# Kernel tuning notes

Measured on AMD Instinct MI355X. Metric: run time of the kernel, lower is better.

Reference implementation:

```python
import jax, jax.numpy as jnp
import numpy as np
from jax import lax

EPS = 1e-5

def _layernorm(x, g, b):
    m = x.mean(-1, keepdims=True)
    v = ((x - m) ** 2).mean(-1, keepdims=True)
    return (x - m) * lax.rsqrt(v + EPS) * g + b

def _batchnorm(x, g, b):
    # x: [N, C, L]; training-mode batch statistics (torch BatchNorm1d default)
    m = x.mean((0, 2), keepdims=True)
    v = ((x - m) ** 2).mean((0, 2), keepdims=True)
    return (x - m) * lax.rsqrt(v + EPS) * g[None, :, None] + b[None, :, None]

def _conv1d(x, w, bias, stride):
    y = lax.conv_general_dilated(x, w, window_strides=(stride,), padding='VALID',
                                 dimension_numbers=('NCH', 'OIH', 'NCH'))
    return y + bias[None, :, None]

def setup_inputs() -> dict:
    key = jax.random.key(0)
    ks = jax.random.split(key, 22)
    B, C, L = 512, 12, 5000
    NF, HID, LAT = 32, 64, 32
    def w(k, shape, fan_in):
        return jax.random.normal(k, shape, jnp.float32) * (1.0 / np.sqrt(fan_in))
    return {
        'x': jax.random.normal(ks[0], (B, C, L), jnp.float32),
        'c1w': w(ks[1], (32, C, 50), C * 50), 'c1b': jnp.zeros((32,), jnp.float32),
        'bn1g': jnp.ones((32,), jnp.float32), 'bn1b': jnp.zeros((32,), jnp.float32),
        'c2w': w(ks[2], (NF, 32, 25), 32 * 25), 'c2b': jnp.zeros((NF,), jnp.float32),
        'bn2g': jnp.ones((NF,), jnp.float32), 'bn2b': jnp.zeros((NF,), jnp.float32),
        'Wi': w(ks[3], (LAT, NF), NF) * 0.5, 'bi': jnp.zeros((LAT,), jnp.float32),
        'ln1g': jnp.ones((LAT,), jnp.float32), 'ln1b': jnp.zeros((LAT,), jnp.float32),
        'Wh': w(ks[4], (HID, LAT), LAT) * 0.5, 'bh': jnp.zeros((HID,), jnp.float32),
        'ln2g': jnp.ones((HID,), jnp.float32), 'ln2b': jnp.zeros((HID,), jnp.float32),
        'Wr': w(ks[5], (LAT, HID), HID) * 0.5, 'br': jnp.zeros((LAT,), jnp.float32),
        'Wo': w(ks[6], (LAT, LAT), LAT), 'bo': jnp.zeros((LAT,), jnp.float32),
    }

def reference(x, c1w, c1b, bn1g, bn1b, c2w, c2b, bn2g, bn2b,
              Wi, bi, ln1g, ln1b, Wh, bh, ln2g, ln2b, Wr, br, Wo, bo):
    # CNN front-end: [B,12,5000] -> [B,32,496] -> [B,32,95]
    h = jax.nn.relu(_batchnorm(_conv1d(x, c1w, c1b, 10), bn1g, bn1b))
    h = jax.nn.relu(_batchnorm(_conv1d(h, c2w, c2b, 5), bn2g, bn2b))
    feats = h.transpose(2, 0, 1)  # [T, B, NF]
    # input_proj + ln1 have no dependence on the recurrent state -> hoist out of loop
    xt_all = _layernorm(jnp.einsum('tbf,lf->tbl', feats, Wi) + bi, ln1g, ln1b)  # [T,B,LAT]

    def step(hstate, xt):
        combined = xt + hstate
        hp = jax.nn.relu(combined @ Wh.T + bh)      # [B, HID]
        hp = _layernorm(hp, ln2g, ln2b)
        hnew = jnp.tanh(hp @ Wr.T + br)             # [B, LAT]
        return hnew, hnew

    h0 = jnp.zeros((x.shape[0], Wr.shape[0]), x.dtype)
    _, outs = lax.scan(step, h0, xt_all)            # outs: [T, B, LAT]
    pooled = outs.mean(0)                           # mean over time
    return pooled @ Wo.T + bo                       # [B, LAT]
```

## Files before the change

### kernel.cpp

```cpp
#include <hip/hip_runtime.h>

#define EPS 1e-5f

#define B    512
#define C_IN 12
#define L_IN 5000
#define C1   32
#define L1   496
#define NF   32
#define L2   95
#define LAT  32
#define HID  64
#define T    L2

typedef short s16x8 __attribute__((ext_vector_type(8)));
typedef float f32x16 __attribute__((ext_vector_type(16)));

__device__ __forceinline__ ushort f2bf(float f) {
    uint u = __builtin_bit_cast(uint, f);
    u += 0x7fff + ((u >> 16) & 1);
    return (ushort)(u >> 16);
}
__device__ __forceinline__ float bf2f(ushort h) {
    return __builtin_bit_cast(float, (uint)h << 16);
}
__device__ __forceinline__ uint pk(float f) {
    ushort h = f2bf(f);
    return (uint)h | ((uint)f2bf(f - bf2f(h)) << 16);
}
__device__ __forceinline__ uint4 pack4(float4 d) {
    return make_uint4(pk(d.x), pk(d.y), pk(d.z), pk(d.w));
}

__global__ void k_prep_w(const float* __restrict__ c1w, const float* __restrict__ c2w,
                         ushort* __restrict__ wfrag1, ushort* __restrict__ wfrag2) {
    int i = blockIdx.x * 256 + threadIdx.x;
    if (i < 6144) {
        int lane = i & 63, r = i >> 6;
        int split = r & 1, s = (r >> 1) & 3, c = r >> 3;
        int oc = lane & 31, kbase = s * 16 + (lane >> 5) * 8;
        ushort o8[8];
#pragma unroll
        for (int j = 0; j < 8; ++j) {
            int kk = kbase + j;
            float w = (kk < 50) ? c1w[oc * 600 + c * 50 + kk] : 0.f;
            ushort hb = f2bf(w);
            o8[j] = split ? f2bf(w - bf2f(hb)) : hb;
        }
        ushort4* dst = reinterpret_cast<ushort4*>(wfrag1) + (size_t)i * 2;
        dst[0] = make_ushort4(o8[0], o8[1], o8[2], o8[3]);
        dst[1] = make_ushort4(o8[4], o8[5], o8[6], o8[7]);
    } else if (i < 14336) {
        int j = i - 6144;
        int lane = j & 63, r = j >> 6;
        int split = r & 1, ks = (r >> 1) & 1, c = r >> 2;
        int oc = lane & 31, kbase = ks * 16 + (lane >> 5) * 8;
        ushort o8[8];
#pragma unroll
        for (int jj = 0; jj < 8; ++jj) {
            int kk = kbase + jj;
            float w = (kk < 25) ? c2w[oc * 800 + c * 25 + kk] : 0.f;
            ushort hb = f2bf(w);
            o8[jj] = split ? f2bf(w - bf2f(hb)) : hb;
        }
        ushort4* dst = reinterpret_cast<ushort4*>(wfrag2) + (size_t)j * 2;
        dst[0] = make_ushort4(o8[0], o8[1], o8[2], o8[3]);
        dst[1] = make_ushort4(o8[4], o8[5], o8[6], o8[7]);
    }
}

__device__ __forceinline__ void conv1_compute(const uint (*xs)[1344], const uint4* wf4,
                                              int c0, int c1, int abase, int lane,
                                              f32x16& hh, f32x16& hl, f32x16& lh) {
    for (int c = c0; c < c1; ++c) {
        const uint* xc = xs[c];
        const uint4* wfc = wf4 + (size_t)c * 512 + lane;
#pragma unroll
        for (int s = 0; s < 4; ++s) {
            const int idx = abase + s * 16;
            uint2 p0 = *reinterpret_cast<const uint2*>(&xc[idx]);
            uint2 p1 = *reinterpret_cast<const uint2*>(&xc[idx + 2]);
            uint2 p2 = *reinterpret_cast<const uint2*>(&xc[idx + 4]);
            uint2 p3 = *reinterpret_cast<const uint2*>(&xc[idx + 6]);
            union { s16x8 v; uint u[4]; } ah, al, bh, bl;
            ah.u[0] = __builtin_amdgcn_perm(p0.y, p0.x, 0x05040100u);
            al.u[0] = __builtin_amdgcn_perm(p0.y, p0.x, 0x07060302u);
            ah.u[1] = __builtin_amdgcn_perm(p1.y, p1.x, 0x05040100u);
            al.u[1] = __builtin_amdgcn_perm(p1.y, p1.x, 0x07060302u);
            ah.u[2] = __builtin_amdgcn_perm(p2.y, p2.x, 0x05040100u);
            al.u[2] = __builtin_amdgcn_perm(p2.y, p2.x, 0x07060302u);
            ah.u[3] = __builtin_amdgcn_perm(p3.y, p3.x, 0x05040100u);
            al.u[3] = __builtin_amdgcn_perm(p3.y, p3.x, 0x07060302u);
            uint4 bq = wfc[s * 128];
            uint4 lq = wfc[s * 128 + 64];
            bh.u[0] = bq.x; bh.u[1] = bq.y; bh.u[2] = bq.z; bh.u[3] = bq.w;
            bl.u[0] = lq.x; bl.u[1] = lq.y; bl.u[2] = lq.z; bl.u[3] = lq.w;
            hh = __builtin_amdgcn_mfma_f32_32x32x16_bf16(ah.v, bh.v, hh, 0, 0, 0);
            hl = __builtin_amdgcn_mfma_f32_32x32x16_bf16(ah.v, bl.v, hl, 0, 0, 0);
            lh = __builtin_amdgcn_mfma_f32_32x32x16_bf16(al.v, bh.v, lh, 0, 0, 0);
        }
    }
}

__global__ __launch_bounds__(256) void k_conv1(const float* __restrict__ x,
                                               const ushort* __restrict__ wfrag,
                                               const float* __restrict__ c1b,
                                               float* __restrict__ y1,
                                               float* __restrict__ raw1) {
    __shared__ uint xs[C_IN][1344];
    __shared__ float redS[4][32], redQ[4][32];
    const int chunk = blockIdx.x, b = blockIdx.y, tid = threadIdx.x;
    const int t0 = chunk * 128;
    const int v4max = min(336, (5000 - 10 * t0) >> 2);
    const float4* xb4 = reinterpret_cast<const float4*>(x + (size_t)b * (C_IN * L_IN) + 10 * t0);

    float4 rA[8], rB[8];
#pragma unroll
    for (int i = 0; i < 8; ++i) {
        const int v = tid + i * 256;
        const int c = v / 336, i4 = v - c * 336;
        rA[i] = make_float4(0, 0, 0, 0);
        if (i4 < v4max) rA[i] = xb4[c * 1250 + i4];
    }
#pragma unroll
    for (int i = 0; i < 8; ++i) {
        const int v = tid + 2048 + i * 256;
        const int c = v / 336, i4 = v - c * 336;
        rB[i] = make_float4(0, 0, 0, 0);
        if (v < 4032 && i4 < v4max) rB[i] = xb4[c * 1250 + i4];
    }

    uint4* xs4 = reinterpret_cast<uint4*>(&xs[0][0]);
#pragma unroll
    for (int i = 0; i < 8; ++i) xs4[tid + i * 256] = pack4(rA[i]);
    asm volatile("s_waitcnt lgkmcnt(0)" ::: "memory");
    __builtin_amdgcn_s_barrier();
    __builtin_amdgcn_sched_barrier(0);

    const int lane = tid & 63, wv = tid >> 6;
    const int cl = lane & 31;
    const int kgrp = lane >> 5;
    const int abase = 10 * (wv * 32 + cl) + kgrp * 8;

    f32x16 hh, hl, lh;
#pragma unroll
    for (int i = 0; i < 16; ++i) { hh[i] = 0.f; hl[i] = 0.f; lh[i] = 0.f; }
    const uint4* wf4 = reinterpret_cast<const uint4*>(wfrag);

    conv1_compute(xs, wf4, 0, 6, abase, lane, hh, hl, lh);

#pragma unroll
    for (int i = 0; i < 8; ++i) {
        const int v = tid + 2048 + i * 256;
        if (v < 4032) xs4[v] = pack4(rB[i]);
    }
    asm volatile("s_waitcnt lgkmcnt(0)" ::: "memory");
    __builtin_amdgcn_s_barrier();
    __builtin_amdgcn_sched_barrier(0);

    conv1_compute(xs, wf4, 6, 12, abase, lane, hh, hl, lh);

    const float bias = c1b[cl];
    float sum = 0.f, sq = 0.f;
    float* yb = y1 + ((size_t)b * C1 + cl) * L1;
#pragma unroll
    for (int q = 0; q < 4; ++q) {
        const int trow = t0 + wv * 32 + 8 * q + 4 * kgrp;
        float4 st;
        st.x = hh[4*q+0] + hl[4*q+0] + lh[4*q+0] + bias;
        st.y = hh[4*q+1] + hl[4*q+1] + lh[4*q+1] + bias;
        st.z = hh[4*q+2] + hl[4*q+2] + lh[4*q+2] + bias;
        st.w = hh[4*q+3] + hl[4*q+3] + lh[4*q+3] + bias;
        if (trow < L1) {
            *reinterpret_cast<float4*>(yb + trow) = st;
            sum += st.x + st.y + st.z + st.w;
            sq  += st.x * st.x + st.y * st.y + st.z * st.z + st.w * st.w;
        }
    }
    sum += __shfl_xor(sum, 32);
    sq  += __shfl_xor(sq, 32);
    if (lane < 32) { redS[wv][cl] = sum; redQ[wv][cl] = sq; }
    __syncthreads();
    if (tid < 64) {
        int o = tid & 31, isQ = tid >> 5;
        float v = isQ ? (redQ[0][o] + redQ[1][o] + redQ[2][o] + redQ[3][o])
                      : (redS[0][o] + redS[1][o] + redS[2][o] + redS[3][o]);
        atomicAdd(&raw1[(isQ ? 1024 : 0) + o * 16], v);
    }
}

__global__ __launch_bounds__(192) void k_conv2(const float* __restrict__ y1,
                                               const ushort* __restrict__ wfrag2,
                                               const float* __restrict__ c2b,
                                               const float* __restrict__ raw1,
                                               const float* __restrict__ bn1g,
                                               const float* __restrict__ bn1b,
                                               float* __restrict__ y2,
                                               float* __restrict__ raw2) {
    __shared__ uint xs[C1][512];
    __shared__ float fin[64];
    __shared__ float redS[3][32], redQ[3][32];
    const int b = blockIdx.x, tid = threadIdx.x;

    if (tid < 32) {
        const float cnt = 1.f / (float)(B * L1);
        float mean = raw1[tid * 16] * cnt;
        float var = raw1[1024 + tid * 16] * cnt - mean * mean;
        float sc = bn1g[tid] * rsqrtf(var + EPS);
        fin[tid] = sc;
        fin[32 + tid] = bn1b[tid] - mean * sc;
    }
    __syncthreads();

    const float4* src = reinterpret_cast<const float4*>(y1 + (size_t)b * (C1 * L1));
    for (int v = tid; v < C1 * 128; v += 192) {
        const int c = v >> 7, i4 = v & 127;
        uint4 o = make_uint4(0, 0, 0, 0);
        if (i4 < 124) {
            const float sc = fin[c], sh = fin[32 + c];
            float4 d = src[c * 124 + i4];
            float e0 = fmaxf(fmaf(d.x, sc, sh), 0.f);
            float e1 = fmaxf(fmaf(d.y, sc, sh), 0.f);
            float e2 = fmaxf(fmaf(d.z, sc, sh), 0.f);
            float e3 = fmaxf(fmaf(d.w, sc, sh), 0.f);
            o = make_uint4(pk(e0), pk(e1), pk(e2), pk(e3));
        }
        *reinterpret_cast<uint4*>(&xs[c][4 * i4]) = o;
    }
    __syncthreads();

    const int lane = tid & 63, wv = tid / 64;
    const int cl = lane & 31;
    const int kgrp = lane >> 5;
    const int tbase = 5 * (wv * 32 + cl) + kgrp * 8;

    f32x16 hh, hl, lh;
#pragma unroll
    for (int i = 0; i < 16; ++i) { hh[i] = 0.f; hl[i] = 0.f; lh[i] = 0.f; }
    const uint4* wf4 = reinterpret_cast<const uint4*>(wfrag2);

    for (int c = 0; c < C1; ++c) {
        const uint* xc = xs[c];
        const uint4* wfc = wf4 + (size_t)c * 256 + lane;
#pragma unroll
        for (int ks = 0; ks < 2; ++ks) {
            const int idx = tbase + ks * 16;
            uint u0 = xc[idx + 0], u1 = xc[idx + 1], u2 = xc[idx + 2], u3 = xc[idx + 3];
            uint u4 = xc[idx + 4], u5 = xc[idx + 5], u6 = xc[idx + 6], u7 = xc[idx + 7];
            union { s16x8 v; uint u[4]; } ah, al, bh, bl;
            ah.u[0] = __builtin_amdgcn_perm(u1, u0, 0x05040100u);
            al.u[0] = __builtin_amdgcn_perm(u1, u0, 0x07060302u);
            ah.u[1] = __builtin_amdgcn_perm(u3, u2, 0x05040100u);
            al.u[1] = __builtin_amdgcn_perm(u3, u2, 0x07060302u);
            ah.u[2] = __builtin_amdgcn_perm(u5, u4, 0x05040100u);
            al.u[2] = __builtin_amdgcn_perm(u5, u4, 0x07060302u);
            ah.u[3] = __builtin_amdgcn_perm(u7, u6, 0x05040100u);
            al.u[3] = __builtin_amdgcn_perm(u7, u6, 0x07060302u);
            uint4 bq = wfc[ks * 128];
            uint4 lq = wfc[ks * 128 + 64];
            bh.u[0] = bq.x; bh.u[1] = bq.y; bh.u[2] = bq.z; bh.u[3] = bq.w;
            bl.u[0] = lq.x; bl.u[1] = lq.y; bl.u[2] = lq.z; bl.u[3] = lq.w;
            hh = __builtin_amdgcn_mfma_f32_32x32x16_bf16(ah.v, bh.v, hh, 0, 0, 0);
            hl = __builtin_amdgcn_mfma_f32_32x32x16_bf16(ah.v, bl.v, hl, 0, 0, 0);
            lh = __builtin_amdgcn_mfma_f32_32x32x16_bf16(al.v, bh.v, lh, 0, 0, 0);
        }
    }

    const float bias = c2b[cl];
    float sum = 0.f, sq = 0.f;
#pragma unroll
    for (int q = 0; q < 4; ++q) {
#pragma unroll
        for (int j = 0; j < 4; ++j) {
            const int t = wv * 32 + 8 * q + 4 * kgrp + j;
            const float v = hh[4*q+j] + hl[4*q+j] + lh[4*q+j] + bias;
            if (t < L2) {
                y2[((size_t)b * L2 + t) * NF + cl] = v;
                sum += v; sq += v * v;
            }
        }
    }
    sum += __shfl_xor(sum, 32);
    sq  += __shfl_xor(sq, 32);
    if (lane < 32) { redS[wv][cl] = sum; redQ[wv][cl] = sq; }
    __syncthreads();
    if (tid < 64) {
        int o = tid & 31, isQ = tid >> 5;
        float v = isQ ? (redQ[0][o] + redQ[1][o] + redQ[2][o])
                      : (redS[0][o] + redS[1][o] + redS[2][o]);
        atomicAdd(&raw2[(isQ ? 1024 : 0) + o * 16], v);
    }
}

__global__ __launch_bounds__(256) void k_proj(const float* __restrict__ y2,
                                              const float* __restrict__ raw2,
                                              const float* __restrict__ bn2g,
                                              const float* __restrict__ bn2b,
                                              const float* __restrict__ Wi,
                                              const float* __restrict__ bi,
                                              const float* __restrict__ ln1g,
                                              const float* __restrict__ ln1b,
                                              const float* __restrict__ Wh,
                                              const float* __restrict__ bh,
                                              float* __restrict__ xt2) {
    __shared__ float fin[64];
    if (threadIdx.x < 32) {
        const float cnt = 1.f / (float)(B * L2);
        float mean = raw2[threadIdx.x * 16] * cnt;
        float var = raw2[1024 + threadIdx.x * 16] * cnt - mean * mean;
        float sc = bn2g[threadIdx.x] * rsqrtf(var + EPS);
        fin[threadIdx.x] = sc;
        fin[32 + threadIdx.x] = bn2b[threadIdx.x] - mean * sc;
    }
    __syncthreads();

    const int r = blockIdx.x * 256 + threadIdx.x;
    const int b = r / 95, t = r - b * 95;

    const float4* row = reinterpret_cast<const float4*>(y2 + (size_t)r * NF);
    float u[NF];
#pragma unroll
    for (int f4 = 0; f4 < 8; ++f4) {
        float4 v = row[f4];
        u[4*f4]   = fmaxf(fmaf(v.x, fin[4*f4],   fin[32 + 4*f4]),   0.f);
        u[4*f4+1] = fmaxf(fmaf(v.y, fin[4*f4+1], fin[32 + 4*f4+1]), 0.f);
        u[4*f4+2] = fmaxf(fmaf(v.z, fin[4*f4+2], fin[32 + 4*f4+2]), 0.f);
        u[4*f4+3] = fmaxf(fmaf(v.w, fin[4*f4+3], fin[32 + 4*f4+3]), 0.f);
    }
    float xln[LAT];
    float s = 0.f, q = 0.f;
#pragma unroll
    for (int l = 0; l < LAT; ++l) {
        float a = bi[l];
#pragma unroll
        for (int f = 0; f < NF; ++f) a = fmaf(u[f], Wi[l * NF + f], a);
        xln[l] = a; s += a; q += a * a;
    }
    const float m = s * (1.f / LAT);
    const float inv = rsqrtf(q * (1.f / LAT) - m * m + EPS);
#pragma unroll
    for (int l = 0; l < LAT; ++l) xln[l] = (xln[l] - m) * inv * ln1g[l] + ln1b[l];

    float4* dst = reinterpret_cast<float4*>(xt2 + ((size_t)t * B + b) * HID);
#pragma unroll
    for (int j4 = 0; j4 < 16; ++j4) {
        float4 o4;
        float a0 = bh[4*j4], a1 = bh[4*j4+1], a2 = bh[4*j4+2], a3 = bh[4*j4+3];
#pragma unroll
        for (int l = 0; l < LAT; ++l) {
            float xl = xln[l];
            a0 = fmaf(xl, Wh[(4*j4)   * LAT + l], a0);
            a1 = fmaf(xl, Wh[(4*j4+1) * LAT + l], a1);
            a2 = fmaf(xl, Wh[(4*j4+2) * LAT + l], a2);
            a3 = fmaf(xl, Wh[(4*j4+3) * LAT + l], a3);
        }
        o4.x = a0; o4.y = a1; o4.z = a2; o4.w = a3;
        dst[j4] = o4;
    }
}

__global__ __launch_bounds__(64) void k_rnn(const float* __restrict__ xt2,
                                            const float* __restrict__ Wh,
                                            const float* __restrict__ ln2g,
                                            const float* __restrict__ ln2b,
                                            const float* __restrict__ Wr,
                                            const float* __restrict__ br,
                                            const float* __restrict__ Wo,
                                            const float* __restrict__ bo,
                                            float* __restrict__ out) {
    __shared__ __align__(16) float aS[64];
    __shared__ __align__(16) float hS[32];
    const int lane = threadIdx.x;
    const int b = blockIdx.x;
    const int l = lane & 31;

    float whv[LAT];
#pragma unroll
    for (int i = 0; i < LAT; ++i) whv[i] = Wh[lane * LAT + i];

    float wg[HID];
    float S1 = 0.f, S2 = br[l];
#pragma unroll
    for (int j = 0; j < HID; ++j) {
        float w = Wr[l * HID + j];
        wg[j] = w * ln2g[j];
        S1 += wg[j];
        S2 = fmaf(w, ln2b[j], S2);
    }

    float hfull[LAT];
#pragma unroll
    for (int i = 0; i < LAT; ++i) hfull[i] = 0.f;
    float pooled = 0.f;
    float xq = xt2[(size_t)b * HID + lane];

    for (int t = 0; t < T; ++t) {
        float xq_next = 0.f;
        if (t + 1 < T) xq_next = xt2[((size_t)(t + 1) * B + b) * HID + lane];

        float a0 = xq, a1 = 0.f, a2c = 0.f, a3c = 0.f;
#pragma unroll
        for (int i = 0; i < 8; ++i) {
            a0  = fmaf(hfull[4*i+0], whv[4*i+0], a0);
            a1  = fmaf(hfull[4*i+1], whv[4*i+1], a1);
            a2c = fmaf(hfull[4*i+2], whv[4*i+2], a2c);
            a3c = fmaf(hfull[4*i+3], whv[4*i+3], a3c);
        }
        const float a = fmaxf((a0 + a1) + (a2c + a3c), 0.f);

        aS[lane] = a;
        asm volatile("s_waitcnt lgkmcnt(0)" ::: "memory");

        float d0 = 0.f, d1 = 0.f, d2 = 0.f, d3 = 0.f;
#pragma unroll
        for (int i = 0; i < 16; ++i) {
            float4 v = reinterpret_cast<const float4*>(aS)[i];
            d0 = fmaf(v.x, wg[4*i+0], d0); d1 = fmaf(v.y, wg[4*i+1], d1);
            d2 = fmaf(v.z, wg[4*i+2], d2); d3 = fmaf(v.w, wg[4*i+3], d3);
        }
        float s = a, q = a * a;
#pragma unroll
        for (int off = 32; off >= 1; off >>= 1) { s += __shfl_xor(s, off); q += __shfl_xor(q, off); }
        const float m = s * (1.f / HID);
        const float inv = __builtin_amdgcn_rsqf(q * (1.f / HID) - m * m + EPS);
        const float dot = (d0 + d1) + (d2 + d3);
        const float a2v = fmaf(inv, dot - m * S1, S2);

        const float z = __builtin_amdgcn_exp2f(2.8853900817779268f * a2v);
        const float h = 1.f - 2.f * __builtin_amdgcn_rcpf(z + 1.f);
        pooled += h;

        if (lane < 32) hS[lane] = h;
        asm volatile("s_waitcnt lgkmcnt(0)" ::: "memory");
#pragma unroll
        for (int i = 0; i < 8; ++i) {
            float4 hv = reinterpret_cast<const float4*>(hS)[i];
            hfull[4*i] = hv.x; hfull[4*i+1] = hv.y; hfull[4*i+2] = hv.z; hfull[4*i+3] = hv.w;
        }
        xq = xq_next;
    }
    pooled *= (1.f / T);
    if (lane < 32) aS[lane] = pooled;
    asm volatile("s_waitcnt lgkmcnt(0)" ::: "memory");

    float wov[LAT];
#pragma unroll
    for (int i = 0; i < LAT; ++i) wov[i] = Wo[l * LAT + i];
    float b0 = bo[l], b1 = 0.f, b2 = 0.f, b3 = 0.f;
#pragma unroll
    for (int i = 0; i < 8; ++i) {
        float4 pv = reinterpret_cast<const float4*>(aS)[i];
        b0 = fmaf(pv.x, wov[4*i+0], b0); b1 = fmaf(pv.y, wov[4*i+1], b1);
        b2 = fmaf(pv.z, wov[4*i+2], b2); b3 = fmaf(pv.w, wov[4*i+3], b3);
    }
    if (lane < 32) out[(size_t)b * LAT + l] = (b0 + b1) + (b2 + b3);
}

extern "C" void kernel_launch(void* const* d_in, const int* in_sizes, int n_in,
                              void* d_out, int out_size, void* d_ws, size_t ws_size,
                              hipStream_t stream) {
    const float* x    = (const float*)d_in[0];
    const float* c1w  = (const float*)d_in[1];
    const float* c1b  = (const float*)d_in[2];
    const float* bn1g = (const float*)d_in[3];
    const float* bn1b = (const float*)d_in[4];
    const float* c2w  = (const float*)d_in[5];
    const float* c2b  = (const float*)d_in[6];
    const float* bn2g = (const float*)d_in[7];
    const float* bn2b = (const float*)d_in[8];
    const float* Wi   = (const float*)d_in[9];
    const float* bi   = (const float*)d_in[10];
    const float* ln1g = (const float*)d_in[11];
    const float* ln1b = (const float*)d_in[12];
    const float* Wh   = (const float*)d_in[13];
    const float* bh   = (const float*)d_in[14];
    const float* ln2g = (const float*)d_in[15];
    const float* ln2b = (const float*)d_in[16];
    const float* Wr   = (const float*)d_in[17];
    const float* br   = (const float*)d_in[18];
    const float* Wo   = (const float*)d_in[19];
    const float* bo   = (const float*)d_in[20];

    float* ws = (float*)d_ws;
    float* raw1 = ws;
    float* raw2 = ws + 2048;
    ushort* wfrag1 = (ushort*)(ws + 4096);
    ushort* wfrag2 = (ushort*)(ws + 28672);
    float* y1   = ws + 61440;
    float* y2   = ws + 8187904;
    float* xt2  = y1;
    float* out  = (float*)d_out;

    hipMemsetAsync(raw1, 0, 4096 * sizeof(float), stream);
    k_prep_w<<<56, 256, 0, stream>>>(c1w, c2w, wfrag1, wfrag2);
    k_conv1<<<dim3(4, B), 256, 0, stream>>>(x, wfrag1, c1b, y1, raw1);
    k_conv2<<<B, 192, 0, stream>>>(y1, wfrag2, c2b, raw1, bn1g, bn1b, y2, raw2);
    k_proj<<<190, 256, 0, stream>>>(y2, raw2, bn2g, bn2b, Wi, bi, ln1g, ln1b, Wh, bh, xt2);
    k_rnn<<<B, 64, 0, stream>>>(xt2, Wh, ln2g, ln2b, Wr, br, Wo, bo, out);
}
```

Measured before the change: 257.5 us.

## Split conv input channels across two wave groups with LDS partial-sum reduction

```diff
diff --git a/kernel.cpp b/kernel.cpp
--- a/kernel.cpp
+++ b/kernel.cpp
@@ -70,9 +70,10 @@
 }
 
 __device__ __forceinline__ void conv1_compute(const uint (*xs)[1344], const uint4* wf4,
-                                              int c0, int c1, int abase, int lane,
+                                              int c0, int abase, int lane,
                                               f32x16& hh, f32x16& hl, f32x16& lh) {
-    for (int c = c0; c < c1; ++c) {
+    for (int cc = 0; cc < 6; ++cc) {
+        const int c = c0 + cc;
         const uint* xc = xs[c];
         const uint4* wfc = wf4 + (size_t)c * 512 + lane;
 #pragma unroll
@@ -102,11 +103,11 @@
     }
 }
 
-__global__ __launch_bounds__(256) void k_conv1(const float* __restrict__ x,
-                                               const ushort* __restrict__ wfrag,
-                                               const float* __restrict__ c1b,
-                                               float* __restrict__ y1,
-                                               float* __restrict__ raw1) {
+__global__ __launch_bounds__(512, 4) void k_conv1(const float* __restrict__ x,
+                                                  const ushort* __restrict__ wfrag,
+                                                  const float* __restrict__ c1b,
+                                                  float* __restrict__ y1,
+                                                  float* __restrict__ raw1) {
     __shared__ uint xs[C_IN][1344];
     __shared__ float redS[4][32], redQ[4][32];
     const int chunk = blockIdx.x, b = blockIdx.y, tid = threadIdx.x;
@@ -114,72 +115,76 @@
     const int v4max = min(336, (5000 - 10 * t0) >> 2);
     const float4* xb4 = reinterpret_cast<const float4*>(x + (size_t)b * (C_IN * L_IN) + 10 * t0);
 
-    float4 rA[8], rB[8];
-#pragma unroll
-    for (int i = 0; i < 8; ++i) {
-        const int v = tid + i * 256;
-        const int c = v / 336, i4 = v - c * 336;
-        rA[i] = make_float4(0, 0, 0, 0);
-        if (i4 < v4max) rA[i] = xb4[c * 1250 + i4];
-    }
-#pragma unroll
-    for (int i = 0; i < 8; ++i) {
-        const int v = tid + 2048 + i * 256;
-        const int c = v / 336, i4 = v - c * 336;
-        rB[i] = make_float4(0, 0, 0, 0);
-        if (v < 4032 && i4 < v4max) rB[i] = xb4[c * 1250 + i4];
-    }
-
     uint4* xs4 = reinterpret_cast<uint4*>(&xs[0][0]);
 #pragma unroll
-    for (int i = 0; i < 8; ++i) xs4[tid + i * 256] = pack4(rA[i]);
-    asm volatile("s_waitcnt lgkmcnt(0)" ::: "memory");
-    __builtin_amdgcn_s_barrier();
-    __builtin_amdgcn_sched_barrier(0);
+    for (int r = 0; r < 2; ++r) {
+        float4 rg[4];
+#pragma unroll
+        for (int i = 0; i < 4; ++i) {
+            const int v = tid + (r * 4 + i) * 512;
+            const int c = v / 336, i4 = v - c * 336;
+            rg[i] = make_float4(0, 0, 0, 0);
+            if (v < 4032 && i4 < v4max) rg[i] = xb4[c * 1250 + i4];
+        }
+#pragma unroll
+        for (int i = 0; i < 4; ++i) {
+            const int v = tid + (r * 4 + i) * 512;
+            if (v < 4032) xs4[v] = pack4(rg[i]);
+        }
+    }
+    __syncthreads();
 
     const int lane = tid & 63, wv = tid >> 6;
+    const int g = wv >> 2;
+    const int tw = wv & 3;
     const int cl = lane & 31;
     const int kgrp = lane >> 5;
-    const int abase = 10 * (wv * 32 + cl) + kgrp * 8;
+    const int abase = 10 * (tw * 32 + cl) + kgrp * 8;
 
     f32x16 hh, hl, lh;
 #pragma unroll
     for (int i = 0; i < 16; ++i) { hh[i] = 0.f; hl[i] = 0.f; lh[i] = 0.f; }
     const uint4* wf4 = reinterpret_cast<const uint4*>(wfrag);
 
-    conv1_compute(xs, wf4, 0, 6, abase, lane, hh, hl, lh);
-
-#pragma unroll
-    for (int i = 0; i < 8; ++i) {
-        const int v = tid + 2048 + i * 256;
-        if (v < 4032) xs4[v] = pack4(rB[i]);
-    }
-    asm volatile("s_waitcnt lgkmcnt(0)" ::: "memory");
-    __builtin_amdgcn_s_barrier();
-    __builtin_amdgcn_sched_barrier(0);
-
-    conv1_compute(xs, wf4, 6, 12, abase, lane, hh, hl, lh);
-
-    const float bias = c1b[cl];
+    conv1_compute(xs, wf4, g * 6, abase, lane, hh, hl, lh);
+
+    f32x16 tot;
+#pragma unroll
+    for (int i = 0; i < 16; ++i) tot[i] = hh[i] + hl[i] + lh[i];
+
+    __syncthreads();
+    float4* pr = reinterpret_cast<float4*>(&xs[0][0]);
+    if (g == 1) {
+#pragma unroll
+        for (int i4 = 0; i4 < 4; ++i4)
+            pr[tw * 256 + i4 * 64 + lane] =
+                make_float4(tot[4*i4], tot[4*i4+1], tot[4*i4+2], tot[4*i4+3]);
+    }
+    __syncthreads();
+
     float sum = 0.f, sq = 0.f;
-    float* yb = y1 + ((size_t)b * C1 + cl) * L1;
-#pragma unroll
-    for (int q = 0; q < 4; ++q) {
-        const int trow = t0 + wv * 32 + 8 * q + 4 * kgrp;
-        float4 st;
-        st.x = hh[4*q+0] + hl[4*q+0] + lh[4*q+0] + bias;
-        st.y = hh[4*q+1] + hl[4*q+1] + lh[4*q+1] + bias;
-        st.z = hh[4*q+2] + hl[4*q+2] + lh[4*q+2] + bias;
-        st.w = hh[4*q+3] + hl[4*q+3] + lh[4*q+3] + bias;
-        if (trow < L1) {
-            *reinterpret_cast<float4*>(yb + trow) = st;
-            sum += st.x + st.y + st.z + st.w;
-            sq  += st.x * st.x + st.y * st.y + st.z * st.z + st.w * st.w;
-        }
-    }
-    sum += __shfl_xor(sum, 32);
-    sq  += __shfl_xor(sq, 32);
-    if (lane < 32) { redS[wv][cl] = sum; redQ[wv][cl] = sq; }
+    if (g == 0) {
+        const float bias = c1b[cl];
+        float* yb = y1 + ((size_t)b * C1 + cl) * L1;
+#pragma unroll
+        for (int q = 0; q < 4; ++q) {
+            float4 p = pr[tw * 256 + q * 64 + lane];
+            const int trow = t0 + tw * 32 + 8 * q + 4 * kgrp;
+            float4 st;
+            st.x = tot[4*q+0] + p.x + bias;
+            st.y = tot[4*q+1] + p.y + bias;
+            st.z = tot[4*q+2] + p.z + bias;
+            st.w = tot[4*q+3] + p.w + bias;
+            if (trow < L1) {
+                *reinterpret_cast<float4*>(yb + trow) = st;
+                sum += st.x + st.y + st.z + st.w;
+                sq  += st.x * st.x + st.y * st.y + st.z * st.z + st.w * st.w;
+            }
+        }
+        sum += __shfl_xor(sum, 32);
+        sq  += __shfl_xor(sq, 32);
+        if (lane < 32) { redS[tw][cl] = sum; redQ[tw][cl] = sq; }
+    }
     __syncthreads();
     if (tid < 64) {
         int o = tid & 31, isQ = tid >> 5;
@@ -189,14 +194,14 @@
     }
 }
 
-__global__ __launch_bounds__(192) void k_conv2(const float* __restrict__ y1,
-                                               const ushort* __restrict__ wfrag2,
-                                               const float* __restrict__ c2b,
-                                               const float* __restrict__ raw1,
-                                               const float* __restrict__ bn1g,
-                                               const float* __restrict__ bn1b,
-                                               float* __restrict__ y2,
-                                               float* __restrict__ raw2) {
+__global__ __launch_bounds__(384, 3) void k_conv2(const float* __restrict__ y1,
+                                                  const ushort* __restrict__ wfrag2,
+                                                  const float* __restrict__ c2b,
+                                                  const float* __restrict__ raw1,
+                                                  const float* __restrict__ bn1g,
+                                                  const float* __restrict__ bn1b,
+                                                  float* __restrict__ y2,
+                                                  float* __restrict__ raw2) {
     __shared__ uint xs[C1][512];
     __shared__ float fin[64];
     __shared__ float redS[3][32], redQ[3][32];
@@ -213,7 +218,7 @@
     __syncthreads();
 
     const float4* src = reinterpret_cast<const float4*>(y1 + (size_t)b * (C1 * L1));
-    for (int v = tid; v < C1 * 128; v += 192) {
+    for (int v = tid; v < C1 * 128; v += 384) {
         const int c = v >> 7, i4 = v & 127;
         uint4 o = make_uint4(0, 0, 0, 0);
         if (i4 < 124) {
@@ -229,17 +234,20 @@
     }
     __syncthreads();
 
-    const int lane = tid & 63, wv = tid / 64;
+    const int lane = tid & 63, wv = tid >> 6;
+    const int g = (wv >= 3) ? 1 : 0;
+    const int tw = wv - 3 * g;
     const int cl = lane & 31;
     const int kgrp = lane >> 5;
-    const int tbase = 5 * (wv * 32 + cl) + kgrp * 8;
+    const int tbase = 5 * (tw * 32 + cl) + kgrp * 8;
 
     f32x16 hh, hl, lh;
 #pragma unroll
     for (int i = 0; i < 16; ++i) { hh[i] = 0.f; hl[i] = 0.f; lh[i] = 0.f; }
     const uint4* wf4 = reinterpret_cast<const uint4*>(wfrag2);
 
-    for (int c = 0; c < C1; ++c) {
+    for (int cc = 0; cc < 16; ++cc) {
+        const int c = g * 16 + cc;
         const uint* xc = xs[c];
         const uint4* wfc = wf4 + (size_t)c * 256 + lane;
 #pragma unroll
@@ -266,23 +274,41 @@
         }
     }
 
-    const float bias = c2b[cl];
+    f32x16 tot;
+#pragma unroll
+    for (int i = 0; i < 16; ++i) tot[i] = hh[i] + hl[i] + lh[i];
+
+    __syncthreads();
+    float4* pr = reinterpret_cast<float4*>(&xs[0][0]);
+    if (g == 1) {
+#pragma unroll
+        for (int i4 = 0; i4 < 4; ++i4)
+            pr[tw * 256 + i4 * 64 + lane] =
+                make_float4(tot[4*i4], tot[4*i4+1], tot[4*i4+2], tot[4*i4+3]);
+    }
+    __syncthreads();
+
     float sum = 0.f, sq = 0.f;
-#pragma unroll
-    for (int q = 0; q < 4; ++q) {
-#pragma unroll
-        for (int j = 0; j < 4; ++j) {
-            const int t = wv * 32 + 8 * q + 4 * kgrp + j;
-            const float v = hh[4*q+j] + hl[4*q+j] + lh[4*q+j] + bias;
-            if (t < L2) {
-                y2[((size_t)b * L2 + t) * NF + cl] = v;
-                sum += v; sq += v * v;
+    if (g == 0) {
+        const float bias = c2b[cl];
+#pragma unroll
+        for (int q = 0; q < 4; ++q) {
+            float4 p = pr[tw * 256 + q * 64 + lane];
+            float v4[4] = { tot[4*q+0] + p.x + bias, tot[4*q+1] + p.y + bias,
+                            tot[4*q+2] + p.z + bias, tot[4*q+3] + p.w + bias };
+#pragma unroll
+            for (int j = 0; j < 4; ++j) {
+                const int t = tw * 32 + 8 * q + 4 * kgrp + j;
+                if (t < L2) {
+                    y2[((size_t)b * L2 + t) * NF + cl] = v4[j];
+                    sum += v4[j]; sq += v4[j] * v4[j];
+                }
             }
         }
-    }
-    sum += __shfl_xor(sum, 32);
-    sq  += __shfl_xor(sq, 32);
-    if (lane < 32) { redS[wv][cl] = sum; redQ[wv][cl] = sq; }
+        sum += __shfl_xor(sum, 32);
+        sq  += __shfl_xor(sq, 32);
+        if (lane < 32) { redS[tw][cl] = sum; redQ[tw][cl] = sq; }
+    }
     __syncthreads();
     if (tid < 64) {
         int o = tid & 31, isQ = tid >> 5;
@@ -493,8 +519,8 @@
 
     hipMemsetAsync(raw1, 0, 4096 * sizeof(float), stream);
     k_prep_w<<<56, 256, 0, stream>>>(c1w, c2w, wfrag1, wfrag2);
-    k_conv1<<<dim3(4, B), 256, 0, stream>>>(x, wfrag1, c1b, y1, raw1);
-    k_conv2<<<B, 192, 0, stream>>>(y1, wfrag2, c2b, raw1, bn1g, bn1b, y2, raw2);
+    k_conv1<<<dim3(4, B), 512, 0, stream>>>(x, wfrag1, c1b, y1, raw1);
+    k_conv2<<<B, 384, 0, stream>>>(y1, wfrag2, c2b, raw1, bn1g, bn1b, y2, raw2);
     k_proj<<<190, 256, 0, stream>>>(y2, raw2, bn2g, bn2b, Wi, bi, ln1g, ln1b, Wh, bh, xt2);
     k_rnn<<<B, 64, 0, stream>>>(xt2, Wh, ln2g, ln2b, Wr, br, Wo, bo, out);
 }
```

New measurement: 228.8 us. -11.2%, faster.
